# Performance work log

Measured on AMD Instinct MI355X. Metric: run time of the kernel, lower is better.

## Reference

```python
import jax, jax.numpy as jnp
import numpy as np

B, N, D, H, TV, COND, BLK = 2, 1024, 1024, 16, 256, 1024, 16
HD = D // H  # 64
S = 2 * N    # total sequence [xt|x0]
EPS = 1e-5


def _ln(x, w):
    # bd3lm LayerNorm: no bias, weight multiply after normalization
    mu = jnp.mean(x, axis=-1, keepdims=True)
    var = jnp.mean(jnp.square(x - mu), axis=-1, keepdims=True)
    return (x - mu) * jax.lax.rsqrt(var + EPS) * w


def _rotate_half(u):
    u1, u2 = jnp.split(u, 2, axis=-1)
    return jnp.concatenate([-u2, u1], axis=-1)


def _apply_rotary(qkv, cos, sin):
    # qkv: (B, n, 3, H, HD); cos/sin: (1, n, 3, 1, HD) with identity on the v slot
    return qkv * cos + _rotate_half(qkv) * sin


def setup_inputs() -> dict:
    key = jax.random.key(0)
    ks = jax.random.split(key, 20)
    inp = {}
    inp['x'] = jax.random.normal(ks[0], (B, S, D), jnp.float32)
    inp['c'] = jax.random.normal(ks[1], (B, COND), jnp.float32)
    inp['encoder_out'] = jax.random.normal(ks[2], (B, TV, D), jnp.float32)
    # encoder padding mask: True = valid
    lengths = jax.random.randint(ks[3], (B,), TV // 2, TV + 1)
    inp['encoder_mask'] = jnp.arange(TV)[None, :] < lengths[:, None]
    # BD3LM block-causal mask over [xt|x0], shape (2N, 2N)
    bt = jnp.arange(N) // BLK
    M11 = bt[:, None] == bt[None, :]   # xt attends xt within same block
    M12 = bt[None, :] < bt[:, None]    # xt attends x0 of strictly earlier blocks
    M21 = jnp.zeros((N, N), bool)      # x0 does not attend xt
    M22 = bt[None, :] <= bt[:, None]   # x0 attends x0 block-causally
    inp['mask'] = jnp.concatenate([
        jnp.concatenate([M11, M12], axis=1),
        jnp.concatenate([M21, M22], axis=1)], axis=0)
    # rotary tables (SEDD-style), identity on v slot
    inv_freq = 1.0 / (10000.0 ** (jnp.arange(0, HD, 2, dtype=jnp.float32) / HD))
    freqs = jnp.outer(jnp.arange(N, dtype=jnp.float32), inv_freq)  # (N, HD/2)
    emb = jnp.concatenate([freqs, freqs], axis=-1)                 # (N, HD)
    cqk, sqk = jnp.cos(emb), jnp.sin(emb)
    inp['cos'] = jnp.stack([cqk, cqk, jnp.ones_like(cqk)], axis=1)[None, :, :, None, :]
    inp['sin'] = jnp.stack([sqk, sqk, jnp.zeros_like(sqk)], axis=1)[None, :, :, None, :]
    # parameters (torch Linear convention: W is (out, in), y = x @ W.T)
    sc = 0.02
    inp['ln1_w'] = jnp.ones((D,), jnp.float32)
    inp['W_qkv'] = jax.random.normal(ks[4], (3 * D, D), jnp.float32) * sc
    inp['W_attn_out'] = jax.random.normal(ks[5], (D, D), jnp.float32) * sc
    inp['ca_ln_w'] = jnp.ones((D,), jnp.float32)
    inp['ca_Wq'] = jax.random.normal(ks[6], (D, D), jnp.float32) * sc
    inp['ca_Wkv'] = jax.random.normal(ks[7], (2 * D, D), jnp.float32) * sc
    inp['ca_Wo'] = jax.random.normal(ks[8], (D, D), jnp.float32) * sc
    inp['ln2_w'] = jnp.ones((D,), jnp.float32)
    inp['W_mlp1'] = jax.random.normal(ks[9], (4 * D, D), jnp.float32) * sc
    inp['b_mlp1'] = jnp.zeros((4 * D,), jnp.float32)
    inp['W_mlp2'] = jax.random.normal(ks[10], (D, 4 * D), jnp.float32) * sc
    inp['b_mlp2'] = jnp.zeros((D,), jnp.float32)
    # adaLN (zero-init in the module; use small random weights for a non-trivial baseline)
    inp['W_ada'] = jax.random.normal(ks[11], (6 * D, COND), jnp.float32) * sc
    inp['b_ada'] = jax.random.normal(ks[12], (6 * D,), jnp.float32) * sc
    return inp


def _forward(x, c, encoder_out, encoder_mask, mask, cos, sin, ln1_w, W_qkv,
             W_attn_out, ca_ln_w, ca_Wq, ca_Wkv, ca_Wo, ln2_w, W_mlp1, b_mlp1,
             W_mlp2, b_mlp2, W_ada, b_ada):
    inv_sqrt_d = 1.0 / jnp.sqrt(jnp.float32(HD))
    ada = c @ W_ada.T + b_ada
    sh_msa, sc_msa, g_msa, sh_mlp, sc_mlp, g_mlp = [
        a[:, None, :] for a in jnp.split(ada, 6, axis=-1)]
    x_skip = x
    x_norm = _ln(x, ln1_w) * (1.0 + sc_msa) + sh_msa
    # qkv + rotary applied separately to xt and x0 halves (same positions 0..N-1)
    qkv = (x_norm @ W_qkv.T).reshape(B, S, 3, H, HD)
    qkv = jnp.concatenate([
        _apply_rotary(qkv[:, :N], cos, sin),
        _apply_rotary(qkv[:, N:], cos, sin)], axis=1)
    q, k, v = qkv[:, :, 0], qkv[:, :, 1], qkv[:, :, 2]  # (B, S, H, HD)
    # block-causal self-attention
    scores = jnp.einsum('bqhd,bkhd->bhqk', q, k) * inv_sqrt_d
    scores = jnp.where(mask[None, None, :, :], scores, jnp.finfo(scores.dtype).min)
    attn = jax.nn.softmax(scores, axis=-1)
    x_attn = jnp.einsum('bhqk,bkhd->bqhd', attn, v).reshape(B, S, D)
    # fused bias-dropout-add-scale (inference: scale * x + residual)
    x = g_msa * (x_attn @ W_attn_out.T) + x_skip
    # cross-attention to visual features
    res = x
    xn = _ln(x, ca_ln_w)
    qc = (xn @ ca_Wq.T).reshape(B, S, H, HD)
    kv = (encoder_out @ ca_Wkv.T).reshape(B, TV, 2, H, HD)
    kc, vc = kv[:, :, 0], kv[:, :, 1]
    cs = jnp.einsum('bqhd,bkhd->bhqk', qc, kc) * inv_sqrt_d
    cs = jnp.where(encoder_mask[:, None, None, :], cs, jnp.finfo(cs.dtype).min)
    ca = jax.nn.softmax(cs, axis=-1)
    co = jnp.einsum('bhqk,bkhd->bqhd', ca, vc).reshape(B, S, D)
    x = res + co @ ca_Wo.T
    # adaLN-modulated MLP (GELU tanh)
    h = _ln(x, ln2_w) * (1.0 + sc_mlp) + sh_mlp
    h = jax.nn.gelu(h @ W_mlp1.T + b_mlp1, approximate=True)
    return g_mlp * (h @ W_mlp2.T + b_mlp2) + x


def reference(x, c, encoder_out, encoder_mask, mask, cos, sin, ln1_w, W_qkv,
              W_attn_out, ca_ln_w, ca_Wq, ca_Wkv, ca_Wo, ln2_w, W_mlp1, b_mlp1,
              W_mlp2, b_mlp2, W_ada, b_ada):
    return _forward(x, c, encoder_out, encoder_mask, mask, cos, sin, ln1_w,
                    W_qkv, W_attn_out, ca_ln_w, ca_Wq, ca_Wkv, ca_Wo, ln2_w,
                    W_mlp1, b_mlp1, W_mlp2, b_mlp2, W_ada, b_ada)
```

## Files before the change

kernel.cpp:

```cpp
#include <hip/hip_runtime.h>
#include <hip/hip_bf16.h>

typedef __bf16 bf16x8 __attribute__((ext_vector_type(8)));
typedef __bf16 bf16x4 __attribute__((ext_vector_type(4)));
typedef __bf16 bf16x2 __attribute__((ext_vector_type(2)));
typedef float f32x4 __attribute__((ext_vector_type(4)));

typedef const __attribute__((address_space(1))) unsigned int* gas_t;
typedef __attribute__((address_space(3))) unsigned int* las_t;

__device__ __forceinline__ void gl_lds16(const void* g, void* l) {
    __builtin_amdgcn_global_load_lds((gas_t)g, (las_t)l, 16, 0, 0);
}

__device__ __forceinline__ float gelu_f(float u) {
    return u / (1.f + __expf(-1.5957691216057308f * (u + 0.044715f * u * u * u)));
}

struct CastArgs {
    const float4* src[8];
    __bf16* dst[8];
    int n4[8];
};
__global__ __launch_bounds__(256) void castmulti(CastArgs a) {
    int seg = blockIdx.y;
    const float4* src = a.src[seg];
    __bf16* dst = a.dst[seg];
    int n4 = a.n4[seg];
    for (int i = blockIdx.x * 256 + threadIdx.x; i < n4; i += 512 * 256) {
        float4 v = src[i];
        bf16x4 o;
        o[0] = (__bf16)v.x; o[1] = (__bf16)v.y; o[2] = (__bf16)v.z; o[3] = (__bf16)v.w;
        *(bf16x4*)(dst + (size_t)i * 4) = o;
    }
}

__global__ __launch_bounds__(256) void ada_kernel(const float* __restrict__ c, const float* __restrict__ W,
                                                  const float* __restrict__ bias, float* __restrict__ ada) {
    int o = blockIdx.x * 4 + (threadIdx.x >> 6);
    int lane = threadIdx.x & 63;
    int b = o / 6144, n = o % 6144;
    const float* cr = c + b * 1024;
    const float* wr = W + (size_t)n * 1024;
    float s = 0.f;
    #pragma unroll
    for (int i = 0; i < 16; ++i) s += cr[lane + i * 64] * wr[lane + i * 64];
    #pragma unroll
    for (int off = 1; off < 64; off <<= 1) s += __shfl_xor(s, off, 64);
    if (lane == 0) ada[o] = s + bias[n];
}

__global__ __launch_bounds__(256) void ln_kernel(const float* __restrict__ x, const float* __restrict__ w,
                                                 const float* __restrict__ ada, int sc_off, int sh_off,
                                                 int has_mod, __bf16* __restrict__ out) {
    int m = blockIdx.x;
    int b = m >> 11;
    int t = threadIdx.x;
    const float* xr = x + (size_t)m * 1024;
    float4 v = *(const float4*)(xr + t * 4);
    float s = v.x + v.y + v.z + v.w;
    float sq = v.x * v.x + v.y * v.y + v.z * v.z + v.w * v.w;
    #pragma unroll
    for (int off = 1; off < 64; off <<= 1) { s += __shfl_xor(s, off, 64); sq += __shfl_xor(sq, off, 64); }
    __shared__ float red[8];
    int wv = t >> 6, lane = t & 63;
    if (lane == 0) { red[wv] = s; red[4 + wv] = sq; }
    __syncthreads();
    s = red[0] + red[1] + red[2] + red[3];
    sq = red[4] + red[5] + red[6] + red[7];
    float mu = s * (1.f / 1024.f);
    float var = sq * (1.f / 1024.f) - mu * mu;
    float rs = rsqrtf(var + 1e-5f);
    const float* sc = ada + b * 6144 + sc_off;
    const float* sh = ada + b * 6144 + sh_off;
    float vv[4] = {v.x, v.y, v.z, v.w};
    #pragma unroll
    for (int i = 0; i < 4; ++i) {
        int d = t * 4 + i;
        float val = (vv[i] - mu) * rs * w[d];
        if (has_mod) val = val * (1.f + sc[d]) + sh[d];
        out[(size_t)m * 1024 + d] = (__bf16)val;
    }
}

__global__ __launch_bounds__(512) void gemm512(
    const __bf16* __restrict__ A, const __bf16* __restrict__ Bw,
    void* __restrict__ Cout, float* __restrict__ part,
    int M, int N, int K, int ksplit,
    const float* __restrict__ bias,
    const float* __restrict__ gate,
    const float* __restrict__ resid,
    int do_gelu, int out_bf16, float scale,
    const float* __restrict__ cosp, const float* __restrict__ sinp,
    __bf16* __restrict__ rq, __bf16* __restrict__ rk, __bf16* __restrict__ rv_,
    int rot) {
    __shared__ __align__(16) __bf16 As[128 * 32];
    __shared__ __align__(16) __bf16 Bs[128 * 32];
    int t = threadIdx.x;
    int wv = t >> 6, lane = t & 63;
    int lrow = lane & 15, quad = lane >> 4;
    int m0 = blockIdx.y * 128, n0 = blockIdx.x * 128;
    int Ks = K / ksplit;
    int kbase = blockIdx.z * Ks;
    int wm = (wv >> 1) * 32, wn = (wv & 1) * 64;
    f32x4 acc[2][4] = {};
    const __bf16* Ag = A + (size_t)(m0 + wv * 16 + (lane >> 2)) * K + kbase + (lane & 3) * 8;
    const __bf16* Bg = Bw + (size_t)(n0 + wv * 16 + (lane >> 2)) * K + kbase + (lane & 3) * 8;
    __bf16* Asw = As + wv * 512;
    __bf16* Bsw = Bs + wv * 512;
    for (int k0 = 0; k0 < Ks; k0 += 32) {
        gl_lds16(Ag + k0, Asw);
        gl_lds16(Bg + k0, Bsw);
        __syncthreads();
        bf16x8 af[2], bfr[4];
        #pragma unroll
        for (int i = 0; i < 2; ++i) af[i] = *(const bf16x8*)(As + (wm + i * 16 + lrow) * 32 + quad * 8);
        #pragma unroll
        for (int j = 0; j < 4; ++j) bfr[j] = *(const bf16x8*)(Bs + (wn + j * 16 + lrow) * 32 + quad * 8);
        #pragma unroll
        for (int i = 0; i < 2; ++i)
            #pragma unroll
            for (int j = 0; j < 4; ++j)
                acc[i][j] = __builtin_amdgcn_mfma_f32_16x16x32_bf16(af[i], bfr[j], acc[i][j], 0, 0, 0);
        __syncthreads();
    }
    if (rot == 1) {
        #pragma unroll
        for (int i = 0; i < 2; ++i)
            #pragma unroll
            for (int j = 0; j < 4; ++j)
                #pragma unroll
                for (int r = 0; r < 4; ++r) {
                    int gm = m0 + wm + i * 16 + quad * 4 + r;
                    int gn = n0 + wn + j * 16 + lrow;
                    int tt = gn >> 10, hd = gn & 1023;
                    int hh = hd >> 6, d = hd & 63;
                    int bb = gm >> 11, s = gm & 2047, p = s & 1023;
                    float val = acc[i][j][r];
                    if (tt < 2) {
                        float cs = cosp[p * 192 + tt * 64 + d];
                        float sn = sinp[p * 192 + tt * 64 + d];
                        float prt = acc[i][j ^ 2][r];
                        float rvv = (d < 32) ? -prt : prt;
                        val = val * cs + rvv * sn;
                        if (tt == 0) val *= 0.125f;
                    }
                    __bf16* dst = (tt == 0) ? rq : (tt == 1) ? rk : rv_;
                    dst[((size_t)(bb * 16 + hh) * 2048 + s) * 64 + d] = (__bf16)val;
                }
        return;
    }
    if (rot == 2) {
        #pragma unroll
        for (int i = 0; i < 2; ++i)
            #pragma unroll
            for (int j = 0; j < 4; ++j)
                #pragma unroll
                for (int r = 0; r < 4; ++r) {
                    int gm = m0 + wm + i * 16 + quad * 4 + r;
                    int gn = n0 + wn + j * 16 + lrow;
                    int bb = gm >> 8, tv = gm & 255;
                    int tt = gn >> 10, hd = gn & 1023;
                    int hh = hd >> 6, d = hd & 63;
                    __bf16* dst = (tt == 0) ? rq : rk;
                    dst[((size_t)(bb * 16 + hh) * 256 + tv) * 64 + d] = (__bf16)acc[i][j][r];
                }
        return;
    }
    if (rot == 3) {
        #pragma unroll
        for (int i = 0; i < 2; ++i)
            #pragma unroll
            for (int j = 0; j < 4; ++j)
                #pragma unroll
                for (int r = 0; r < 4; ++r) {
                    int gm = m0 + wm + i * 16 + quad * 4 + r;
                    int gn = n0 + wn + j * 16 + lrow;
                    int bb = gm >> 11, s = gm & 2047;
                    int hh = gn >> 6, d = gn & 63;
                    rq[((size_t)(bb * 16 + hh) * 2048 + s) * 64 + d] = (__bf16)(acc[i][j][r] * scale);
                }
        return;
    }
    if (ksplit > 1) {
        float* pp = part + (size_t)blockIdx.z * M * N;
        #pragma unroll
        for (int i = 0; i < 2; ++i)
            #pragma unroll
            for (int j = 0; j < 4; ++j)
                #pragma unroll
                for (int r = 0; r < 4; ++r) {
                    int gm = m0 + wm + i * 16 + quad * 4 + r;
                    int gn = n0 + wn + j * 16 + lrow;
                    pp[(size_t)gm * N + gn] = acc[i][j][r] * scale;
                }
        return;
    }
    #pragma unroll
    for (int i = 0; i < 2; ++i) {
        #pragma unroll
        for (int j = 0; j < 4; ++j) {
            #pragma unroll
            for (int r = 0; r < 4; ++r) {
                int gm = m0 + wm + i * 16 + quad * 4 + r;
                int gn = n0 + wn + j * 16 + lrow;
                float val = acc[i][j][r] * scale;
                if (bias) val += bias[gn];
                if (do_gelu) val = gelu_f(val);
                if (gate) val *= gate[(gm >> 11) * 6144 + gn];
                if (resid) val += resid[(size_t)gm * N + gn];
                if (out_bf16) ((__bf16*)Cout)[(size_t)gm * N + gn] = (__bf16)val;
                else ((float*)Cout)[(size_t)gm * N + gn] = val;
            }
        }
    }
}

__global__ __launch_bounds__(256) void reduce2(
    const float4* __restrict__ p0, const float4* __restrict__ p1,
    const float* __restrict__ bias, const float* __restrict__ gate,
    const float* __restrict__ resid, float* __restrict__ out, int n4tot) {
    int i = blockIdx.x * 256 + threadIdx.x;
    if (i >= n4tot) return;
    float4 a = p0[i], b = p1[i];
    int idx = i * 4;
    int n = idx & 1023;
    int bb = idx >> 21;
    float4 bs = *(const float4*)(bias + n);
    float4 g = *(const float4*)(gate + bb * 6144 + n);
    float4 rr = ((const float4*)resid)[i];
    float4 o;
    o.x = g.x * (a.x + b.x + bs.x) + rr.x;
    o.y = g.y * (a.y + b.y + bs.y) + rr.y;
    o.z = g.z * (a.z + b.z + bs.z) + rr.z;
    o.w = g.w * (a.w + b.w + bs.w) + rr.w;
    ((float4*)out)[i] = o;
}

__global__ __launch_bounds__(256) void attn_kernel(
    const __bf16* __restrict__ qp, const __bf16* __restrict__ kp, const __bf16* __restrict__ vp,
    __bf16* __restrict__ op, const void* __restrict__ emask, int Sk, int mode) {
    __shared__ __align__(16) __bf16 Ks[2][64][72];
    __shared__ __align__(16) __bf16 Vt[2][64][72];
    __shared__ __align__(16) __bf16 Ps[4][16][72];
    __shared__ __align__(16) float Msk[256];
    int bh = blockIdx.y;
    int b = bh >> 4, h = bh & 15;
    int s0 = blockIdx.x * 64;
    int t = threadIdx.x;
    int wv = t >> 6, lane = t & 63;
    int lrow = lane & 15, quad = lane >> 4;
    const __bf16* qbase = qp + ((size_t)(b * 16 + h) * 2048) * 64;
    const __bf16* kbase = kp + ((size_t)(b * 16 + h) * Sk) * 64;
    const __bf16* vbase = vp + ((size_t)(b * 16 + h) * Sk) * 64;

    const __bf16* qrow = qbase + (size_t)(s0 + wv * 16 + lrow) * 64;
    bf16x8 bq0 = *(const bf16x8*)(qrow + quad * 8);
    bf16x8 bq1 = *(const bf16x8*)(qrow + 32 + quad * 8);

    if (mode == 1) {
        bool i32 = (((const unsigned char*)emask)[1] == 0);
        int kg = t & 255;
        bool vis = i32 ? (((const int*)emask)[b * Sk + kg] != 0)
                       : (((const unsigned char*)emask)[b * Sk + kg] != 0);
        Msk[kg] = vis ? 0.f : -1e30f;
    }

    int qg = s0 + wv * 16 + lrow;
    bool qh = qg < 1024;
    int qb1 = qg >> 4, qb2 = (qg - 1024) >> 4;

    int nt;
    if (mode == 1) nt = Sk >> 6;
    else nt = (s0 < 1024) ? (s0 / 64 + 2) : ((s0 - 1024) / 64 + 1);

    auto tile_kb = [&](int ti) -> int {
        if (mode == 1) return ti * 64;
        if (s0 < 1024) return (ti == 0) ? s0 : 1024 + (ti - 1) * 64;
        return 1024 + ti * 64;
    };

    int r0 = t >> 3, c0 = t & 7;
    int vj = (t & 31) * 2, vd = t >> 5;

    uint4 ka0, ka1;
    bf16x8 va0, va1;
    auto load_regs = [&](int kb) {
        ka0 = *(const uint4*)(kbase + (size_t)(kb + r0) * 64 + c0 * 8);
        ka1 = *(const uint4*)(kbase + (size_t)(kb + r0 + 32) * 64 + c0 * 8);
        va0 = *(const bf16x8*)(vbase + (size_t)(kb + vj) * 64 + vd * 8);
        va1 = *(const bf16x8*)(vbase + (size_t)(kb + vj + 1) * 64 + vd * 8);
    };
    auto write_lds = [&](int bb) {
        *(uint4*)(&Ks[bb][r0][c0 * 8]) = ka0;
        *(uint4*)(&Ks[bb][r0 + 32][c0 * 8]) = ka1;
        #pragma unroll
        for (int i = 0; i < 8; ++i) {
            bf16x2 pr; pr[0] = va0[i]; pr[1] = va1[i];
            *(bf16x2*)(&Vt[bb][vd * 8 + i][vj]) = pr;
        }
    };

    load_regs(tile_kb(0));
    write_lds(0);

    float lsum = 0.f;
    f32x4 oacc[4] = {};
    const float M0 = 10.f;

    for (int ti = 0; ti < nt; ++ti) {
        __syncthreads();
        if (ti + 1 < nt) load_regs(tile_kb(ti + 1));
        int cur = ti & 1;
        int kb = tile_kb(ti);
        f32x4 sacc[4] = {};
        #pragma unroll
        for (int cc = 0; cc < 4; ++cc) {
            bf16x8 ak0 = *(const bf16x8*)(&Ks[cur][cc * 16 + lrow][quad * 8]);
            bf16x8 ak1 = *(const bf16x8*)(&Ks[cur][cc * 16 + lrow][32 + quad * 8]);
            sacc[cc] = __builtin_amdgcn_mfma_f32_16x16x32_bf16(ak0, bq0, sacc[cc], 0, 0, 0);
            sacc[cc] = __builtin_amdgcn_mfma_f32_16x16x32_bf16(ak1, bq1, sacc[cc], 0, 0, 0);
        }
        #pragma unroll
        for (int cc = 0; cc < 4; ++cc) {
            float mx, my, mz, mw;
            if (mode == 1) {
                float4 mb = *(const float4*)(&Msk[kb + cc * 16 + quad * 4]);
                mx = mb.x; my = mb.y; mz = mb.z; mw = mb.w;
            } else {
                bool vis;
                if (kb < 1024) { int kblk = (kb >> 4) + cc; vis = qh && (kblk == qb1); }
                else { int kblk = ((kb - 1024) >> 4) + cc; vis = qh ? (kblk < qb1) : (kblk <= qb2); }
                float mv = vis ? 0.f : -1e30f;
                mx = my = mz = mw = mv;
            }
            float p0 = __expf(sacc[cc][0] + mx - M0);
            float p1 = __expf(sacc[cc][1] + my - M0);
            float p2 = __expf(sacc[cc][2] + mz - M0);
            float p3 = __expf(sacc[cc][3] + mw - M0);
            lsum += (p0 + p1) + (p2 + p3);
            bf16x4 pk;
            pk[0] = (__bf16)p0; pk[1] = (__bf16)p1; pk[2] = (__bf16)p2; pk[3] = (__bf16)p3;
            *(bf16x4*)(&Ps[wv][lrow][cc * 16 + quad * 4]) = pk;
        }
        #pragma unroll
        for (int ks = 0; ks < 64; ks += 32) {
            bf16x8 bp = *(const bf16x8*)(&Ps[wv][lrow][ks + quad * 8]);
            #pragma unroll
            for (int i = 0; i < 4; ++i) {
                bf16x8 av = *(const bf16x8*)(&Vt[cur][i * 16 + lrow][ks + quad * 8]);
                oacc[i] = __builtin_amdgcn_mfma_f32_16x16x32_bf16(av, bp, oacc[i], 0, 0, 0);
            }
        }
        if (ti + 1 < nt) write_lds((ti + 1) & 1);
    }
    lsum += __shfl_xor(lsum, 16, 64);
    lsum += __shfl_xor(lsum, 32, 64);
    float rl = 1.f / lsum;
    __bf16* obase = op + ((size_t)(b * 2048 + qg)) * 1024 + h * 64;
    #pragma unroll
    for (int i = 0; i < 4; ++i) {
        bf16x4 ov;
        #pragma unroll
        for (int r = 0; r < 4; ++r) ov[r] = (__bf16)(oacc[i][r] * rl);
        *(bf16x4*)(obase + i * 16 + quad * 4) = ov;
    }
}


extern "C" void kernel_launch(void* const* d_in, const int* in_sizes, int n_in,
                              void* d_out, int out_size, void* d_ws, size_t ws_size,
                              hipStream_t stream) {
    const float* x      = (const float*)d_in[0];
    const float* c      = (const float*)d_in[1];
    const float* enc    = (const float*)d_in[2];
    const void*  emask  = d_in[3];
    const float* cosp   = (const float*)d_in[5];
    const float* sinp   = (const float*)d_in[6];
    const float* ln1_w  = (const float*)d_in[7];
    const float* W_qkv  = (const float*)d_in[8];
    const float* W_ao   = (const float*)d_in[9];
    const float* ca_ln_w= (const float*)d_in[10];
    const float* ca_Wq  = (const float*)d_in[11];
    const float* ca_Wkv = (const float*)d_in[12];
    const float* ca_Wo  = (const float*)d_in[13];
    const float* ln2_w  = (const float*)d_in[14];
    const float* W_m1   = (const float*)d_in[15];
    const float* b_m1   = (const float*)d_in[16];
    const float* W_m2   = (const float*)d_in[17];
    const float* b_m2   = (const float*)d_in[18];
    const float* W_ada  = (const float*)d_in[19];
    const float* b_ada  = (const float*)d_in[20];
    float* out = (float*)d_out;

    char* ws = (char*)d_ws;
    const size_t MB = 1ull << 20;
    float*  ada   = (float*)(ws + 0);
    __bf16* encb  = (__bf16*)(ws + 1 * MB);
    __bf16* xn    = (__bf16*)(ws + 2 * MB);
    float*  xA    = (float*)(ws + 10 * MB);
    float*  xB    = (float*)(ws + 26 * MB);
    float*  part  = (float*)(ws + 42 * MB);
    __bf16* qb    = (__bf16*)(ws + 74 * MB);
    __bf16* kbuf  = (__bf16*)(ws + 82 * MB);
    __bf16* vbuf  = (__bf16*)(ws + 90 * MB);
    __bf16* xat   = (__bf16*)(ws + 98 * MB);
    __bf16* hbuf  = (__bf16*)(ws + 98 * MB);
    __bf16* wqkv  = (__bf16*)(ws + 130 * MB);
    __bf16* wao   = (__bf16*)(ws + 136 * MB);
    __bf16* wcaq  = (__bf16*)(ws + 138 * MB);
    __bf16* wcakv = (__bf16*)(ws + 140 * MB);
    __bf16* wcao  = (__bf16*)(ws + 144 * MB);
    __bf16* wm1   = (__bf16*)(ws + 146 * MB);
    __bf16* wm2   = (__bf16*)(ws + 154 * MB);
    __bf16* kc    = kbuf;
    __bf16* vc    = kbuf + 524288;

    CastArgs ca;
    ca.src[0] = (const float4*)enc;    ca.dst[0] = encb;  ca.n4[0] = 131072;
    ca.src[1] = (const float4*)W_qkv;  ca.dst[1] = wqkv;  ca.n4[1] = 786432;
    ca.src[2] = (const float4*)W_ao;   ca.dst[2] = wao;   ca.n4[2] = 262144;
    ca.src[3] = (const float4*)ca_Wq;  ca.dst[3] = wcaq;  ca.n4[3] = 262144;
    ca.src[4] = (const float4*)ca_Wkv; ca.dst[4] = wcakv; ca.n4[4] = 524288;
    ca.src[5] = (const float4*)ca_Wo;  ca.dst[5] = wcao;  ca.n4[5] = 262144;
    ca.src[6] = (const float4*)W_m1;   ca.dst[6] = wm1;   ca.n4[6] = 1048576;
    ca.src[7] = (const float4*)W_m2;   ca.dst[7] = wm2;   ca.n4[7] = 1048576;
    castmulti<<<dim3(512, 8), 256, 0, stream>>>(ca);
    ada_kernel<<<3072, 256, 0, stream>>>(c, W_ada, b_ada, ada);
    ln_kernel<<<4096, 256, 0, stream>>>(x, ln1_w, ada, 1024, 0, 1, xn);
    gemm512<<<dim3(24, 32, 1), 512, 0, stream>>>(xn, wqkv, nullptr, nullptr, 4096, 3072, 1024, 1,
        nullptr, nullptr, nullptr, 0, 1, 1.f, cosp, sinp, qb, kbuf, vbuf, 1);
    attn_kernel<<<dim3(32, 32), 256, 0, stream>>>(qb, kbuf, vbuf, xat, nullptr, 2048, 0);
    gemm512<<<dim3(8, 32, 1), 512, 0, stream>>>(xat, wao, xA, nullptr, 4096, 1024, 1024, 1,
        nullptr, ada + 2048, x, 0, 0, 1.f, nullptr, nullptr, nullptr, nullptr, nullptr, 0);
    ln_kernel<<<4096, 256, 0, stream>>>(xA, ca_ln_w, ada, 0, 0, 0, xn);
    gemm512<<<dim3(8, 32, 1), 512, 0, stream>>>(xn, wcaq, nullptr, nullptr, 4096, 1024, 1024, 1,
        nullptr, nullptr, nullptr, 0, 1, 0.125f, nullptr, nullptr, qb, nullptr, nullptr, 3);
    gemm512<<<dim3(16, 4, 1), 512, 0, stream>>>(encb, wcakv, nullptr, nullptr, 512, 2048, 1024, 1,
        nullptr, nullptr, nullptr, 0, 1, 1.f, nullptr, nullptr, kc, vc, nullptr, 2);
    attn_kernel<<<dim3(32, 32), 256, 0, stream>>>(qb, kc, vc, vbuf, emask, 256, 1);
    gemm512<<<dim3(8, 32, 1), 512, 0, stream>>>(vbuf, wcao, xB, nullptr, 4096, 1024, 1024, 1,
        nullptr, nullptr, xA, 0, 0, 1.f, nullptr, nullptr, nullptr, nullptr, nullptr, 0);
    ln_kernel<<<4096, 256, 0, stream>>>(xB, ln2_w, ada, 4096, 3072, 1, xn);
    gemm512<<<dim3(32, 32, 1), 512, 0, stream>>>(xn, wm1, hbuf, nullptr, 4096, 4096, 1024, 1,
        b_m1, nullptr, nullptr, 1, 1, 1.f, nullptr, nullptr, nullptr, nullptr, nullptr, 0);
    gemm512<<<dim3(8, 32, 2), 512, 0, stream>>>(hbuf, wm2, nullptr, part, 4096, 1024, 4096, 2,
        nullptr, nullptr, nullptr, 0, 0, 1.f, nullptr, nullptr, nullptr, nullptr, nullptr, 0);
    reduce2<<<4096, 256, 0, stream>>>((const float4*)part, (const float4*)(part + (size_t)4096 * 1024),
        b_m2, ada + 5120, xB, out, 1048576);
}
```

Before: 569.6 us.

## Use 4-wave 64x64-per-wave GEMM for QKV/MLP1 and 128-query attention blocks

After: 581.9 us. +2.2%, slower.

```diff
diff --git a/kernel.cpp b/kernel.cpp
--- a/kernel.cpp
+++ b/kernel.cpp
@@ -83,14 +83,10 @@
     }
 }
 
-__global__ __launch_bounds__(512) void gemm512(
+__global__ __launch_bounds__(256) void gemm256(
     const __bf16* __restrict__ A, const __bf16* __restrict__ Bw,
-    void* __restrict__ Cout, float* __restrict__ part,
-    int M, int N, int K, int ksplit,
-    const float* __restrict__ bias,
-    const float* __restrict__ gate,
-    const float* __restrict__ resid,
-    int do_gelu, int out_bf16, float scale,
+    void* __restrict__ Cout, int M, int N, int K,
+    const float* __restrict__ bias, int do_gelu, int out_bf16,
     const float* __restrict__ cosp, const float* __restrict__ sinp,
     __bf16* __restrict__ rq, __bf16* __restrict__ rk, __bf16* __restrict__ rv_,
     int rot) {
@@ -100,25 +96,28 @@
     int wv = t >> 6, lane = t & 63;
     int lrow = lane & 15, quad = lane >> 4;
     int m0 = blockIdx.y * 128, n0 = blockIdx.x * 128;
-    int Ks = K / ksplit;
-    int kbase = blockIdx.z * Ks;
-    int wm = (wv >> 1) * 32, wn = (wv & 1) * 64;
-    f32x4 acc[2][4] = {};
-    const __bf16* Ag = A + (size_t)(m0 + wv * 16 + (lane >> 2)) * K + kbase + (lane & 3) * 8;
-    const __bf16* Bg = Bw + (size_t)(n0 + wv * 16 + (lane >> 2)) * K + kbase + (lane & 3) * 8;
-    __bf16* Asw = As + wv * 512;
-    __bf16* Bsw = Bs + wv * 512;
-    for (int k0 = 0; k0 < Ks; k0 += 32) {
-        gl_lds16(Ag + k0, Asw);
-        gl_lds16(Bg + k0, Bsw);
+    int wm = (wv >> 1) * 64, wn = (wv & 1) * 64;
+    f32x4 acc[4][4] = {};
+    const __bf16* Ag = A + (size_t)(m0 + wv * 16 + (lane >> 2)) * K + (lane & 3) * 8;
+    const __bf16* Bg = Bw + (size_t)(n0 + wv * 16 + (lane >> 2)) * K + (lane & 3) * 8;
+    __bf16* Asw0 = As + wv * 512;
+    __bf16* Asw1 = As + 2048 + wv * 512;
+    __bf16* Bsw0 = Bs + wv * 512;
+    __bf16* Bsw1 = Bs + 2048 + wv * 512;
+    const size_t rstep = (size_t)64 * K;
+    for (int k0 = 0; k0 < K; k0 += 32) {
+        gl_lds16(Ag + k0, Asw0);
+        gl_lds16(Ag + k0 + rstep, Asw1);
+        gl_lds16(Bg + k0, Bsw0);
+        gl_lds16(Bg + k0 + rstep, Bsw1);
         __syncthreads();
-        bf16x8 af[2], bfr[4];
-        #pragma unroll
-        for (int i = 0; i < 2; ++i) af[i] = *(const bf16x8*)(As + (wm + i * 16 + lrow) * 32 + quad * 8);
+        bf16x8 af[4], bfr[4];
+        #pragma unroll
+        for (int i = 0; i < 4; ++i) af[i] = *(const bf16x8*)(As + (wm + i * 16 + lrow) * 32 + quad * 8);
         #pragma unroll
         for (int j = 0; j < 4; ++j) bfr[j] = *(const bf16x8*)(Bs + (wn + j * 16 + lrow) * 32 + quad * 8);
         #pragma unroll
-        for (int i = 0; i < 2; ++i)
+        for (int i = 0; i < 4; ++i)
             #pragma unroll
             for (int j = 0; j < 4; ++j)
                 acc[i][j] = __builtin_amdgcn_mfma_f32_16x16x32_bf16(af[i], bfr[j], acc[i][j], 0, 0, 0);
@@ -126,7 +125,7 @@
     }
     if (rot == 1) {
         #pragma unroll
-        for (int i = 0; i < 2; ++i)
+        for (int i = 0; i < 4; ++i)
             #pragma unroll
             for (int j = 0; j < 4; ++j)
                 #pragma unroll
@@ -150,6 +149,64 @@
                 }
         return;
     }
+    #pragma unroll
+    for (int i = 0; i < 4; ++i) {
+        #pragma unroll
+        for (int j = 0; j < 4; ++j) {
+            #pragma unroll
+            for (int r = 0; r < 4; ++r) {
+                int gm = m0 + wm + i * 16 + quad * 4 + r;
+                int gn = n0 + wn + j * 16 + lrow;
+                float val = acc[i][j][r];
+                if (bias) val += bias[gn];
+                if (do_gelu) val = gelu_f(val);
+                if (out_bf16) ((__bf16*)Cout)[(size_t)gm * N + gn] = (__bf16)val;
+                else ((float*)Cout)[(size_t)gm * N + gn] = val;
+            }
+        }
+    }
+}
+
+__global__ __launch_bounds__(512) void gemm512(
+    const __bf16* __restrict__ A, const __bf16* __restrict__ Bw,
+    void* __restrict__ Cout, float* __restrict__ part,
+    int M, int N, int K, int ksplit,
+    const float* __restrict__ bias,
+    const float* __restrict__ gate,
+    const float* __restrict__ resid,
+    int do_gelu, int out_bf16, float scale,
+    __bf16* __restrict__ rq, __bf16* __restrict__ rk,
+    int rot) {
+    __shared__ __align__(16) __bf16 As[128 * 32];
+    __shared__ __align__(16) __bf16 Bs[128 * 32];
+    int t = threadIdx.x;
+    int wv = t >> 6, lane = t & 63;
+    int lrow = lane & 15, quad = lane >> 4;
+    int m0 = blockIdx.y * 128, n0 = blockIdx.x * 128;
+    int Ks = K / ksplit;
+    int kbase = blockIdx.z * Ks;
+    int wm = (wv >> 1) * 32, wn = (wv & 1) * 64;
+    f32x4 acc[2][4] = {};
+    const __bf16* Ag = A + (size_t)(m0 + wv * 16 + (lane >> 2)) * K + kbase + (lane & 3) * 8;
+    const __bf16* Bg = Bw + (size_t)(n0 + wv * 16 + (lane >> 2)) * K + kbase + (lane & 3) * 8;
+    __bf16* Asw = As + wv * 512;
+    __bf16* Bsw = Bs + wv * 512;
+    for (int k0 = 0; k0 < Ks; k0 += 32) {
+        gl_lds16(Ag + k0, Asw);
+        gl_lds16(Bg + k0, Bsw);
+        __syncthreads();
+        bf16x8 af[2], bfr[4];
+        #pragma unroll
+        for (int i = 0; i < 2; ++i) af[i] = *(const bf16x8*)(As + (wm + i * 16 + lrow) * 32 + quad * 8);
+        #pragma unroll
+        for (int j = 0; j < 4; ++j) bfr[j] = *(const bf16x8*)(Bs + (wn + j * 16 + lrow) * 32 + quad * 8);
+        #pragma unroll
+        for (int i = 0; i < 2; ++i)
+            #pragma unroll
+            for (int j = 0; j < 4; ++j)
+                acc[i][j] = __builtin_amdgcn_mfma_f32_16x16x32_bf16(af[i], bfr[j], acc[i][j], 0, 0, 0);
+        __syncthreads();
+    }
     if (rot == 2) {
         #pragma unroll
         for (int i = 0; i < 2; ++i)
@@ -237,16 +294,16 @@
     ((float4*)out)[i] = o;
 }
 
-__global__ __launch_bounds__(256) void attn_kernel(
+__global__ __launch_bounds__(512) void attn_kernel(
     const __bf16* __restrict__ qp, const __bf16* __restrict__ kp, const __bf16* __restrict__ vp,
     __bf16* __restrict__ op, const void* __restrict__ emask, int Sk, int mode) {
     __shared__ __align__(16) __bf16 Ks[2][64][72];
     __shared__ __align__(16) __bf16 Vt[2][64][72];
-    __shared__ __align__(16) __bf16 Ps[4][16][72];
+    __shared__ __align__(16) __bf16 Ps[8][16][72];
     __shared__ __align__(16) float Msk[256];
     int bh = blockIdx.y;
     int b = bh >> 4, h = bh & 15;
-    int s0 = blockIdx.x * 64;
+    int s0 = blockIdx.x * 128;
     int t = threadIdx.x;
     int wv = t >> 6, lane = t & 63;
     int lrow = lane & 15, quad = lane >> 4;
@@ -258,12 +315,11 @@
     bf16x8 bq0 = *(const bf16x8*)(qrow + quad * 8);
     bf16x8 bq1 = *(const bf16x8*)(qrow + 32 + quad * 8);
 
-    if (mode == 1) {
+    if (mode == 1 && t < 256) {
         bool i32 = (((const unsigned char*)emask)[1] == 0);
-        int kg = t & 255;
-        bool vis = i32 ? (((const int*)emask)[b * Sk + kg] != 0)
-                       : (((const unsigned char*)emask)[b * Sk + kg] != 0);
-        Msk[kg] = vis ? 0.f : -1e30f;
+        bool vis = i32 ? (((const int*)emask)[b * Sk + t] != 0)
+                       : (((const unsigned char*)emask)[b * Sk + t] != 0);
+        Msk[t] = vis ? 0.f : -1e30f;
     }
 
     int qg = s0 + wv * 16 + lrow;
@@ -272,32 +328,36 @@
 
     int nt;
     if (mode == 1) nt = Sk >> 6;
-    else nt = (s0 < 1024) ? (s0 / 64 + 2) : ((s0 - 1024) / 64 + 1);
+    else if (s0 < 1024) nt = s0 / 64 + 4;
+    else nt = (s0 - 1024) / 64 + 2;
 
     auto tile_kb = [&](int ti) -> int {
         if (mode == 1) return ti * 64;
-        if (s0 < 1024) return (ti == 0) ? s0 : 1024 + (ti - 1) * 64;
+        if (s0 < 1024) return (ti < 2) ? (s0 + ti * 64) : (1024 + (ti - 2) * 64);
         return 1024 + ti * 64;
     };
 
     int r0 = t >> 3, c0 = t & 7;
-    int vj = (t & 31) * 2, vd = t >> 5;
-
-    uint4 ka0, ka1;
+    int vj = (t & 31) * 2, vd = (t >> 5) & 7;
+    bool doV = t < 256;
+
+    uint4 ka;
     bf16x8 va0, va1;
     auto load_regs = [&](int kb) {
-        ka0 = *(const uint4*)(kbase + (size_t)(kb + r0) * 64 + c0 * 8);
-        ka1 = *(const uint4*)(kbase + (size_t)(kb + r0 + 32) * 64 + c0 * 8);
-        va0 = *(const bf16x8*)(vbase + (size_t)(kb + vj) * 64 + vd * 8);
-        va1 = *(const bf16x8*)(vbase + (size_t)(kb + vj + 1) * 64 + vd * 8);
+        ka = *(const uint4*)(kbase + (size_t)(kb + r0) * 64 + c0 * 8);
+        if (doV) {
+            va0 = *(const bf16x8*)(vbase + (size_t)(kb + vj) * 64 + vd * 8);
+            va1 = *(const bf16x8*)(vbase + (size_t)(kb + vj + 1) * 64 + vd * 8);
+        }
     };
     auto write_lds = [&](int bb) {
-        *(uint4*)(&Ks[bb][r0][c0 * 8]) = ka0;
-        *(uint4*)(&Ks[bb][r0 + 32][c0 * 8]) = ka1;
-        #pragma unroll
-        for (int i = 0; i < 8; ++i) {
-            bf16x2 pr; pr[0] = va0[i]; pr[1] = va1[i];
-            *(bf16x2*)(&Vt[bb][vd * 8 + i][vj]) = pr;
+        *(uint4*)(&Ks[bb][r0][c0 * 8]) = ka;
+        if (doV) {
+            #pragma unroll
+            for (int i = 0; i < 8; ++i) {
+                bf16x2 pr; pr[0] = va0[i]; pr[1] = va1[i];
+                *(bf16x2*)(&Vt[bb][vd * 8 + i][vj]) = pr;
+            }
         }
     };
 
@@ -428,24 +488,24 @@
     castmulti<<<dim3(512, 8), 256, 0, stream>>>(ca);
     ada_kernel<<<3072, 256, 0, stream>>>(c, W_ada, b_ada, ada);
     ln_kernel<<<4096, 256, 0, stream>>>(x, ln1_w, ada, 1024, 0, 1, xn);
-    gemm512<<<dim3(24, 32, 1), 512, 0, stream>>>(xn, wqkv, nullptr, nullptr, 4096, 3072, 1024, 1,
-        nullptr, nullptr, nullptr, 0, 1, 1.f, cosp, sinp, qb, kbuf, vbuf, 1);
-    attn_kernel<<<dim3(32, 32), 256, 0, stream>>>(qb, kbuf, vbuf, xat, nullptr, 2048, 0);
+    gemm256<<<dim3(24, 32), 256, 0, stream>>>(xn, wqkv, nullptr, 4096, 3072, 1024,
+        nullptr, 0, 1, cosp, sinp, qb, kbuf, vbuf, 1);
+    attn_kernel<<<dim3(16, 32), 512, 0, stream>>>(qb, kbuf, vbuf, xat, nullptr, 2048, 0);
     gemm512<<<dim3(8, 32, 1), 512, 0, stream>>>(xat, wao, xA, nullptr, 4096, 1024, 1024, 1,
-        nullptr, ada + 2048, x, 0, 0, 1.f, nullptr, nullptr, nullptr, nullptr, nullptr, 0);
+        nullptr, ada + 2048, x, 0, 0, 1.f, nullptr, nullptr, 0);
     ln_kernel<<<4096, 256, 0, stream>>>(xA, ca_ln_w, ada, 0, 0, 0, xn);
     gemm512<<<dim3(8, 32, 1), 512, 0, stream>>>(xn, wcaq, nullptr, nullptr, 4096, 1024, 1024, 1,
-        nullptr, nullptr, nullptr, 0, 1, 0.125f, nullptr, nullptr, qb, nullptr, nullptr, 3);
+        nullptr, nullptr, nullptr, 0, 1, 0.125f, qb, nullptr, 3);
     gemm512<<<dim3(16, 4, 1), 512, 0, stream>>>(encb, wcakv, nullptr, nullptr, 512, 2048, 1024, 1,
-        nullptr, nullptr, nullptr, 0, 1, 1.f, nullptr, nullptr, kc, vc, nullptr, 2);
-    attn_kernel<<<dim3(32, 32), 256, 0, stream>>>(qb, kc, vc, vbuf, emask, 256, 1);
+        nullptr, nullptr, nullptr, 0, 1, 1.f, kc, vc, 2);
+    attn_kernel<<<dim3(16, 32), 512, 0, stream>>>(qb, kc, vc, vbuf, emask, 256, 1);
     gemm512<<<dim3(8, 32, 1), 512, 0, stream>>>(vbuf, wcao, xB, nullptr, 4096, 1024, 1024, 1,
-        nullptr, nullptr, xA, 0, 0, 1.f, nullptr, nullptr, nullptr, nullptr, nullptr, 0);
+        nullptr, nullptr, xA, 0, 0, 1.f, nullptr, nullptr, 0);
     ln_kernel<<<4096, 256, 0, stream>>>(xB, ln2_w, ada, 4096, 3072, 1, xn);
-    gemm512<<<dim3(32, 32, 1), 512, 0, stream>>>(xn, wm1, hbuf, nullptr, 4096, 4096, 1024, 1,
-        b_m1, nullptr, nullptr, 1, 1, 1.f, nullptr, nullptr, nullptr, nullptr, nullptr, 0);
+    gemm256<<<dim3(32, 32), 256, 0, stream>>>(xn, wm1, hbuf, 4096, 4096, 1024,
+        b_m1, 1, 1, nullptr, nullptr, nullptr, nullptr, nullptr, 0);
     gemm512<<<dim3(8, 32, 2), 512, 0, stream>>>(hbuf, wm2, nullptr, part, 4096, 1024, 4096, 2,
-        nullptr, nullptr, nullptr, 0, 0, 1.f, nullptr, nullptr, nullptr, nullptr, nullptr, 0);
+        nullptr, nullptr, nullptr, 0, 0, 1.f, nullptr, nullptr, 0);
     reduce2<<<4096, 256, 0, stream>>>((const float4*)part, (const float4*)(part + (size_t)4096 * 1024),
         b_m2, ada + 5120, xB, out, 1048576);
 }
```
